# Kernel optimization log

Hardware: AMD Instinct MI355X
Metric: run time of the kernel (lower is better)

Reference implementation:

```python
import jax, jax.numpy as jnp
import numpy as np

B, S, D = 32, 512, 512
H, DH = 8, 64          # head_num, att_embedding_size
DFF = 4 * D
NEG = float(-2**32 + 1)
LN_EPS = 1e-3          # keras LayerNormalization default


def layer_norm(x, gamma, beta):
    mu = jnp.mean(x, axis=-1, keepdims=True)
    var = jnp.mean(jnp.square(x - mu), axis=-1, keepdims=True)
    return (x - mu) / jnp.sqrt(var + LN_EPS) * gamma + beta


def setup_inputs() -> dict:
    key = jax.random.key(0)
    ks = jax.random.split(key, 10)
    queries = jax.random.normal(ks[0], (B, S, D), dtype=jnp.float32)
    keys = jax.random.normal(ks[1], (B, S, D), dtype=jnp.float32)
    query_lens = jax.random.randint(ks[2], (B, 1), 1, S + 1)
    key_lens = jax.random.randint(ks[3], (B, 1), 1, S + 1)
    # learned params (TruncatedNormal stddev 0.05-ish / Glorot approximated by scaled normals)
    W_Q = jax.random.normal(ks[4], (D, D), dtype=jnp.float32) * 0.05
    W_K = jax.random.normal(ks[5], (D, D), dtype=jnp.float32) * 0.05
    W_V = jax.random.normal(ks[6], (D, D), dtype=jnp.float32) * 0.05
    fw1 = jax.random.normal(ks[7], (D, DFF), dtype=jnp.float32) * (1.0 / np.sqrt(D))
    fw2 = jax.random.normal(ks[8], (DFF, D), dtype=jnp.float32) * (1.0 / np.sqrt(DFF))
    ln_gamma = jnp.ones((D,), dtype=jnp.float32)
    ln_beta = jnp.zeros((D,), dtype=jnp.float32)
    return {"queries": queries, "keys": keys, "W_Q": W_Q, "W_K": W_K, "W_V": W_V,
            "fw1": fw1, "fw2": fw2, "ln_gamma": ln_gamma, "ln_beta": ln_beta,
            "query_lens": query_lens, "key_lens": key_lens}


def reference(queries, keys, W_Q, W_K, W_V, fw1, fw2, ln_gamma, ln_beta, query_lens, key_lens):
    # masks from sequence lengths: [B, S] float {0,1}
    pos = jnp.arange(S)
    q_mask = (pos[None, :] < query_lens).astype(queries.dtype)  # [B,S]
    k_mask = (pos[None, :] < key_lens).astype(queries.dtype)    # [B,S]

    # QKV projections, split into heads: [B,S,H,DH]
    Q = (queries @ W_Q).reshape(B, S, H, DH)
    Kp = (keys @ W_K).reshape(B, S, H, DH)
    V = (keys @ W_V).reshape(B, S, H, DH)

    # scaled dot-product scores: [B,H,Sq,Sk]
    scores = jnp.einsum('bqhd,bkhd->bhqk', Q, Kp) / jnp.sqrt(jnp.asarray(DH, queries.dtype))

    # key padding mask
    scores = jnp.where(k_mask[:, None, None, :] == 1, scores, NEG)
    # blinding: kill the diagonal (self-position)
    eye = jnp.eye(S, dtype=bool)
    scores = jnp.where(eye[None, None, :, :], NEG, scores)

    scores = scores - jnp.max(scores, axis=-1, keepdims=True)
    attn = jax.nn.softmax(scores, axis=-1)
    # query mask zeros out padded query rows (after softmax, as in source)
    attn = attn * q_mask[:, None, :, None]

    out = jnp.einsum('bhqk,bkhd->bqhd', attn, V).reshape(B, S, D)

    result = out + queries                       # use_res
    result = layer_norm(result, ln_gamma, ln_beta)  # shared ln (use_layer_norm)

    # feed-forward
    h = jax.nn.relu(result @ fw1) @ fw2
    result = result + h
    result = layer_norm(result, ln_gamma, ln_beta)

    # output_type == 'mean'
    return jnp.mean(result, axis=1, keepdims=True)  # [B,1,D]
```

## Files before the change

### kernel.cpp

```cpp
#include <hip/hip_runtime.h>

typedef unsigned short ushort_t;
typedef unsigned int uint_t;
typedef __attribute__((ext_vector_type(4))) float f32x4;
typedef __attribute__((ext_vector_type(2))) float f32x2;
typedef __attribute__((ext_vector_type(8))) short s16x8;
typedef __attribute__((ext_vector_type(8))) _Float16 f16x8;
typedef __attribute__((ext_vector_type(4))) unsigned short u16x4;

#define NEGV -60000.0f

__device__ __forceinline__ ushort_t f2bf(float f) {
  unsigned int u = __builtin_bit_cast(unsigned int, f);
  return (ushort_t)((u + 0x7fffu + ((u >> 16) & 1u)) >> 16);
}
__device__ __forceinline__ float bf2f(ushort_t h) {
  unsigned int u = ((unsigned int)h) << 16;
  return __builtin_bit_cast(float, u);
}
__device__ __forceinline__ void gload_lds16(const void* g, void* l) {
  __builtin_amdgcn_global_load_lds(
      (const __attribute__((address_space(1))) unsigned int*)g,
      (__attribute__((address_space(3))) unsigned int*)l, 16, 0, 0);
}

template<int EPI>
__global__ __launch_bounds__(256)
void gemm_bt(const ushort_t* __restrict__ A, const ushort_t* __restrict__ A2,
             int lda,
             const ushort_t* __restrict__ Bt, int ldb,
             void* __restrict__ Cv, int ldc, int K,
             long long sB, long long sC)
{
  __shared__ ushort_t As[128 * 32];
  __shared__ ushort_t Bs[128 * 32];

  const int tid = threadIdx.x;
  const int w = tid >> 6;
  const int lane = tid & 63;
  const int z = blockIdx.z;

  const ushort_t* Az = (z == 0) ? A : A2;
  const ushort_t* Bz = Bt + (size_t)z * sB;

  const int orig = blockIdx.x + gridDim.x * blockIdx.y;
  const int bx = (orig >> 3) % gridDim.x;
  const int by = (orig & 7) + 8 * ((orig >> 3) / gridDim.x);
  const int m0 = by * 128;
  const int n0 = bx * 128;

  const int wm = (w >> 1) * 64;
  const int wn = (w & 1) * 64;

  f32x4 acc[4][4];
#pragma unroll
  for (int m = 0; m < 4; ++m)
#pragma unroll
    for (int n = 0; n < 4; ++n)
      acc[m][n] = (f32x4){0.f, 0.f, 0.f, 0.f};

  const int cA0 = w * 64 + lane;
  const int cA1 = 256 + cA0;

  const int nk = K >> 5;
  for (int kt = 0; kt < nk; ++kt) {
    const int k0 = kt << 5;
    gload_lds16(Az + (size_t)(m0 + (cA0 >> 2)) * lda + (k0 + (cA0 & 3) * 8),
                As + (size_t)(w * 64) * 8);
    gload_lds16(Az + (size_t)(m0 + (cA1 >> 2)) * lda + (k0 + (cA1 & 3) * 8),
                As + (size_t)(256 + w * 64) * 8);
    gload_lds16(Bz + (size_t)(n0 + (cA0 >> 2)) * ldb + (k0 + (cA0 & 3) * 8),
                Bs + (size_t)(w * 64) * 8);
    gload_lds16(Bz + (size_t)(n0 + (cA1 >> 2)) * ldb + (k0 + (cA1 & 3) * 8),
                Bs + (size_t)(256 + w * 64) * 8);
    __syncthreads();

    s16x8 af[4], bfr[4];
#pragma unroll
    for (int m = 0; m < 4; ++m)
      af[m] = *(const s16x8*)(As + (size_t)(wm + m * 16 + (lane & 15)) * 32 +
                              ((lane >> 4) * 8));
#pragma unroll
    for (int n = 0; n < 4; ++n)
      bfr[n] = *(const s16x8*)(Bs + (size_t)(wn + n * 16 + (lane & 15)) * 32 +
                               ((lane >> 4) * 8));
#pragma unroll
    for (int m = 0; m < 4; ++m)
#pragma unroll
      for (int n = 0; n < 4; ++n)
        acc[m][n] = __builtin_amdgcn_mfma_f32_16x16x32_bf16(af[m], bfr[n],
                                                            acc[m][n], 0, 0, 0);
    __syncthreads();
  }

  const float s0 = (EPI == 4 && z == 0) ? 0.125f : 1.0f;
  char* Cz = (char*)Cv + (size_t)sC * z;
  const int r_base = (lane >> 4) * 4;
  const int c_base = lane & 15;
#pragma unroll
  for (int m = 0; m < 4; ++m)
#pragma unroll
    for (int n = 0; n < 4; ++n)
#pragma unroll
      for (int j = 0; j < 4; ++j) {
        const int rg = m0 + wm + m * 16 + r_base + j;
        const int cg = n0 + wn + n * 16 + c_base;
        float v = acc[m][n][j];
        const size_t idx = (size_t)rg * ldc + cg;
        if constexpr (EPI == 0) {
          ((float*)Cz)[idx] = v;
        } else if constexpr (EPI == 2) {
          ((ushort_t*)Cz)[idx] = f2bf(fmaxf(v, 0.f));
        } else {
          ((ushort_t*)Cz)[idx] = f2bf(v * s0);
        }
      }
}

__global__ __launch_bounds__(256, 3)
void flash_attn(const ushort_t* __restrict__ Qg, const ushort_t* __restrict__ Kg,
                const ushort_t* __restrict__ Vt, ushort_t* __restrict__ AOb,
                const int* __restrict__ qlen, const int* __restrict__ klen)
{
  __shared__ ushort_t sm[24576];
  ushort_t* PQ = sm + 16384;

  const int tid = threadIdx.x, w = tid >> 6, lane = tid & 63;
  const int fr = lane & 15, fq = lane >> 4;

  int id = blockIdx.x;
  id = (id & 7) * 128 + (id >> 3);
  const int qt = id & 3, h = (id >> 2) & 7, b = id >> 5;
  const int q0 = qt * 128;
  const int KL = klen[b], QL = qlen[b];

  if (q0 >= QL) {
#pragma unroll
    for (int i = 0; i < 8; ++i) {
      int idx = i * 256 + tid;
      int rr = idx >> 4, cc = (idx & 15) << 2;
      *(u16x4*)&AOb[((size_t)(b * 512 + q0 + rr)) * 512 + h * 64 + cc] =
          (u16x4){0, 0, 0, 0};
    }
    return;
  }

  int nt = (KL + 63) >> 6;
  if (KL == 1) nt = 8;

  const ushort_t* Qrow = Qg + ((size_t)(b * 512 + q0)) * 512 + h * 64;
  const ushort_t* Krow = Kg + ((size_t)b * 512) * 512 + h * 64;
  const ushort_t* Vrow = Vt + (((size_t)b * 8 + h) * 64) * 512;

#pragma unroll
  for (int i = 0; i < 4; ++i) {
    int s = i * 256 + tid, r = s >> 3, c = (s & 7) ^ (r & 7);
    gload_lds16(Qrow + (size_t)r * 512 + c * 8, PQ + (i * 256 + w * 64) * 8);
  }
#pragma unroll
  for (int i = 0; i < 2; ++i) {
    int s = i * 256 + tid, r = s >> 3, c = (s & 7) ^ (r & 7);
    gload_lds16(Krow + (size_t)r * 512 + c * 8, sm + (i * 256 + w * 64) * 8);
    gload_lds16(Vrow + (size_t)r * 512 + c * 8, sm + 4096 + (i * 256 + w * 64) * 8);
  }
  __syncthreads();

  s16x8 qf[2][2];
#pragma unroll
  for (int m = 0; m < 2; ++m)
#pragma unroll
    for (int kc = 0; kc < 2; ++kc) {
      int r = w * 32 + m * 16 + fr;
      qf[m][kc] = *(const s16x8*)(PQ + r * 64 + (((kc * 4 + fq) ^ (r & 7)) * 8));
    }

  float mrun[2][4], lrun[2][4];
  f32x4 oacc[2][4];
#pragma unroll
  for (int m = 0; m < 2; ++m)
#pragma unroll
    for (int j = 0; j < 4; ++j) { mrun[m][j] = -1e30f; lrun[m][j] = 0.f; }
#pragma unroll
  for (int m = 0; m < 2; ++m)
#pragma unroll
    for (int nd = 0; nd < 4; ++nd)
      oacc[m][nd] = (f32x4){0.f, 0.f, 0.f, 0.f};

  for (int t = 0; t < nt; ++t) {
    ushort_t* Kb = sm + (t & 1) * 8192;
    ushort_t* Vb = Kb + 4096;
    if (t + 1 < nt) {
      const int kv1 = (t + 1) * 64;
      ushort_t* Kn = sm + ((t + 1) & 1) * 8192;
#pragma unroll
      for (int i = 0; i < 2; ++i) {
        int s = i * 256 + tid, r = s >> 3, c = (s & 7) ^ (r & 7);
        gload_lds16(Krow + (size_t)(kv1 + r) * 512 + c * 8,
                    Kn + (i * 256 + w * 64) * 8);
        gload_lds16(Vrow + (size_t)r * 512 + kv1 + c * 8,
                    Kn + 4096 + (i * 256 + w * 64) * 8);
      }
    }
    const int kv0 = t * 64;

    f32x4 sacc[2][4];
#pragma unroll
    for (int m = 0; m < 2; ++m)
#pragma unroll
      for (int n = 0; n < 4; ++n)
        sacc[m][n] = (f32x4){0.f, 0.f, 0.f, 0.f};
#pragma unroll
    for (int n = 0; n < 4; ++n)
#pragma unroll
      for (int kc = 0; kc < 2; ++kc) {
        int r = n * 16 + fr;
        s16x8 kf = *(const s16x8*)(Kb + r * 64 + (((kc * 4 + fq) ^ (r & 7)) * 8));
        sacc[0][n] = __builtin_amdgcn_mfma_f32_16x16x32_bf16(qf[0][kc], kf, sacc[0][n], 0, 0, 0);
        sacc[1][n] = __builtin_amdgcn_mfma_f32_16x16x32_bf16(qf[1][kc], kf, sacc[1][n], 0, 0, 0);
      }

#pragma unroll
    for (int m = 0; m < 2; ++m)
#pragma unroll
      for (int j = 0; j < 4; ++j) {
        const int rl = w * 32 + m * 16 + fq * 4 + j;
        const int rg = q0 + rl;
        float sv[4];
        float tmax = -1e30f;
#pragma unroll
        for (int n = 0; n < 4; ++n) {
          int cg = kv0 + n * 16 + fr;
          float v = sacc[m][n][j];
          if (cg >= KL || cg == rg) v = NEGV;
          sv[n] = v;
          tmax = fmaxf(tmax, v);
        }
#pragma unroll
        for (int o = 1; o < 16; o <<= 1) tmax = fmaxf(tmax, __shfl_xor(tmax, o));
        const float mnew = fmaxf(mrun[m][j], tmax);
        const float sf = __expf(mrun[m][j] - mnew);
        mrun[m][j] = mnew;
        float ps = 0.f;
        _Float16* prow = (_Float16*)(PQ + rl * 64);
#pragma unroll
        for (int n = 0; n < 4; ++n) {
          float p = __expf(sv[n] - mnew);
          ps += p;
          int cl = n * 2 + (fr >> 3);
          prow[((cl ^ (rl & 7)) * 8) + (fr & 7)] = (_Float16)p;
        }
        lrun[m][j] = lrun[m][j] * sf + ps;
#pragma unroll
        for (int nd = 0; nd < 4; ++nd) oacc[m][nd][j] *= sf;
      }

#pragma unroll
    for (int kc = 0; kc < 2; ++kc) {
      s16x8 pf[2];
#pragma unroll
      for (int m = 0; m < 2; ++m) {
        int rl = w * 32 + m * 16 + fr;
        pf[m] = *(const s16x8*)(PQ + rl * 64 + (((kc * 4 + fq) ^ (rl & 7)) * 8));
      }
#pragma unroll
      for (int nd = 0; nd < 4; ++nd) {
        int d = nd * 16 + fr;
        s16x8 vf = *(const s16x8*)(Vb + d * 64 + (((kc * 4 + fq) ^ (d & 7)) * 8));
#pragma unroll
        for (int m = 0; m < 2; ++m)
          oacc[m][nd] = __builtin_amdgcn_mfma_f32_16x16x32_f16(
              __builtin_bit_cast(f16x8, pf[m]), __builtin_bit_cast(f16x8, vf),
              oacc[m][nd], 0, 0, 0);
      }
    }
    __syncthreads();
  }

#pragma unroll
  for (int m = 0; m < 2; ++m)
#pragma unroll
    for (int j = 0; j < 4; ++j) {
      float l = lrun[m][j];
#pragma unroll
      for (int o = 1; o < 16; o <<= 1) l += __shfl_xor(l, o);
      const int rg = q0 + w * 32 + m * 16 + fq * 4 + j;
      const float inv = (rg < QL) ? (1.f / l) : 0.f;
#pragma unroll
      for (int nd = 0; nd < 4; ++nd)
        AOb[((size_t)(b * 512 + rg)) * 512 + h * 64 + nd * 16 + fr] =
            f2bf(oacc[m][nd][j] * inv);
    }
}

__global__ __launch_bounds__(256) void cvt_bf16(const float* __restrict__ in,
                                                ushort_t* __restrict__ out, int n4) {
  int i = blockIdx.x * 256 + threadIdx.x;
  if (i >= n4) return;
  f32x4 v = ((const f32x4*)in)[i];
  u16x4 o;
#pragma unroll
  for (int j = 0; j < 4; ++j) o[j] = f2bf(v[j]);
  ((u16x4*)out)[i] = o;
}

__global__ __launch_bounds__(256) void transpose_cvt(const float* __restrict__ in,
                                                     ushort_t* __restrict__ out,
                                                     int R, int C) {
  __shared__ float tile[32][33];
  const int c0 = blockIdx.x * 32, r0 = blockIdx.y * 32;
  const int tx = threadIdx.x & 31, ty = threadIdx.x >> 5;
#pragma unroll
  for (int i = 0; i < 32; i += 8)
    tile[ty + i][tx] = in[(size_t)(r0 + ty + i) * C + (c0 + tx)];
  __syncthreads();
#pragma unroll
  for (int i = 0; i < 32; i += 8)
    out[(size_t)(c0 + ty + i) * R + (r0 + tx)] = f2bf(tile[tx][ty + i]);
}

__global__ __launch_bounds__(256) void build_vt(const ushort_t* __restrict__ V,
                                                ushort_t* __restrict__ Vt) {
  __shared__ ushort_t tile[64 * 65];
  const int s0 = blockIdx.x * 64, h = blockIdx.y, b = blockIdx.z;
  const int t = threadIdx.x;
#pragma unroll
  for (int i = 0; i < 16; ++i) {
    int idx = i * 256 + t;
    int sl = idx >> 6, d = idx & 63;
    tile[sl * 65 + d] = V[(size_t)(b * 512 + s0 + sl) * 512 + h * 64 + d];
  }
  __syncthreads();
  _Float16* vt = (_Float16*)Vt;
#pragma unroll
  for (int i = 0; i < 16; ++i) {
    int idx = i * 256 + t;
    int d = idx >> 6, sl = idx & 63;
    vt[((size_t)(b * 8 + h) * 64 + d) * 512 + (s0 + sl)] =
        (_Float16)bf2f(tile[sl * 65 + d]);
  }
}

__global__ __launch_bounds__(256) void ln1(const ushort_t* __restrict__ xb,
                                           const float* __restrict__ r,
                                           const float* __restrict__ g,
                                           const float* __restrict__ be,
                                           ushort_t* __restrict__ ob) {
  const int row = blockIdx.x, t = threadIdx.x;
  const size_t base = (size_t)row * 512;
  const uint_t xv = ((const uint_t*)(xb + base))[t];
  const f32x2 rv = ((const f32x2*)(r + base))[t];
  float v0 = bf2f((ushort_t)(xv & 0xffff)) + rv[0];
  float v1 = bf2f((ushort_t)(xv >> 16)) + rv[1];
  float s = v0 + v1, q = v0 * v0 + v1 * v1;
#pragma unroll
  for (int o = 32; o; o >>= 1) { s += __shfl_xor(s, o); q += __shfl_xor(q, o); }
  __shared__ float ps[4], pq[4];
  const int w = t >> 6, lane = t & 63;
  if (lane == 0) { ps[w] = s; pq[w] = q; }
  __syncthreads();
  s = ps[0] + ps[1] + ps[2] + ps[3];
  q = pq[0] + pq[1] + pq[2] + pq[3];
  const float mu = s * 0.001953125f;
  const float var = q * 0.001953125f - mu * mu;
  const float inv = 1.0f / sqrtf(var + 1e-3f);
  const float y0 = (v0 - mu) * inv * g[2 * t] + be[2 * t];
  const float y1 = (v1 - mu) * inv * g[2 * t + 1] + be[2 * t + 1];
  ((uint_t*)(ob + base))[t] = (uint_t)f2bf(y0) | ((uint_t)f2bf(y1) << 16);
}

__global__ __launch_bounds__(256) void ln2(const float* __restrict__ h2a,
                                           const float* __restrict__ h2b,
                                           const ushort_t* __restrict__ r1b,
                                           const float* __restrict__ g,
                                           const float* __restrict__ be,
                                           ushort_t* __restrict__ ob) {
  const int row = blockIdx.x, t = threadIdx.x;
  const size_t base = (size_t)row * 512;
  const f32x2 a = ((const f32x2*)(h2a + base))[t];
  const f32x2 b = ((const f32x2*)(h2b + base))[t];
  const uint_t rv = ((const uint_t*)(r1b + base))[t];
  float v0 = a[0] + b[0] + bf2f((ushort_t)(rv & 0xffff));
  float v1 = a[1] + b[1] + bf2f((ushort_t)(rv >> 16));
  float s = v0 + v1, q = v0 * v0 + v1 * v1;
#pragma unroll
  for (int o = 32; o; o >>= 1) { s += __shfl_xor(s, o); q += __shfl_xor(q, o); }
  __shared__ float ps[4], pq[4];
  const int w = t >> 6, lane = t & 63;
  if (lane == 0) { ps[w] = s; pq[w] = q; }
  __syncthreads();
  s = ps[0] + ps[1] + ps[2] + ps[3];
  q = pq[0] + pq[1] + pq[2] + pq[3];
  const float mu = s * 0.001953125f;
  const float var = q * 0.001953125f - mu * mu;
  const float inv = 1.0f / sqrtf(var + 1e-3f);
  const float y0 = (v0 - mu) * inv * g[2 * t] + be[2 * t];
  const float y1 = (v1 - mu) * inv * g[2 * t + 1] + be[2 * t + 1];
  ((uint_t*)(ob + base))[t] = (uint_t)f2bf(y0) | ((uint_t)f2bf(y1) << 16);
}

__global__ void mean_partial(const ushort_t* __restrict__ r3,
                             float* __restrict__ part) {
  const int sc = blockIdx.x, b = blockIdx.y, d = threadIdx.x;
  float s = 0.f;
#pragma unroll 4
  for (int i = 0; i < 64; ++i)
    s += bf2f(r3[(size_t)(b * 512 + sc * 64 + i) * 512 + d]);
  part[(size_t)(b * 8 + sc) * 512 + d] = s;
}
__global__ void mean_final(const float* __restrict__ part, float* __restrict__ out) {
  const int b = blockIdx.x, d = threadIdx.x;
  float s = 0.f;
#pragma unroll
  for (int i = 0; i < 8; ++i) s += part[(size_t)(b * 8 + i) * 512 + d];
  out[b * 512 + d] = s * (1.0f / 512.0f);
}

extern "C" void kernel_launch(void* const* d_in, const int* in_sizes, int n_in,
                              void* d_out, int out_size, void* d_ws, size_t ws_size,
                              hipStream_t stream) {
  (void)in_sizes; (void)n_in; (void)out_size; (void)ws_size;
  const float* queries = (const float*)d_in[0];
  const float* keys    = (const float*)d_in[1];
  const float* W_Q = (const float*)d_in[2];
  const float* W_K = (const float*)d_in[3];
  const float* W_V = (const float*)d_in[4];
  const float* fw1 = (const float*)d_in[5];
  const float* fw2 = (const float*)d_in[6];
  const float* ln_g = (const float*)d_in[7];
  const float* ln_b = (const float*)d_in[8];
  const int* qlen = (const int*)d_in[9];
  const int* klen = (const int*)d_in[10];
  float* out = (float*)d_out;

  char* ws = (char*)d_ws;
  const size_t MB = 1048576;
  ushort_t* XQ  = (ushort_t*)(ws + 0 * MB);
  ushort_t* XK  = (ushort_t*)(ws + 16 * MB);
  ushort_t* Qb  = (ushort_t*)(ws + 32 * MB);
  ushort_t* Vb  = (ushort_t*)(ws + 64 * MB);
  ushort_t* VT  = (ushort_t*)(ws + 80 * MB);
  ushort_t* AOb = (ushort_t*)(ws + 96 * MB);
  ushort_t* R1B = (ushort_t*)(ws + 112 * MB);
  ushort_t* H1  = (ushort_t*)(ws + 0 * MB);
  float*    H2  = (float*)(ws + 128 * MB);
  ushort_t* R3B = (ushort_t*)(ws + 192 * MB);
  char*     wsw = ws + 208 * MB;
  ushort_t* WQT  = (ushort_t*)(wsw);
  ushort_t* FW1T = (ushort_t*)(wsw + 3 * 524288);
  ushort_t* FW2T = (ushort_t*)(wsw + 3 * 524288 + 2097152);
  float*    PART = (float*)(wsw + 3 * 524288 + 2 * 2097152);

  cvt_bf16<<<8192, 256, 0, stream>>>(queries, XQ, 2097152);
  cvt_bf16<<<8192, 256, 0, stream>>>(keys, XK, 2097152);
  transpose_cvt<<<dim3(16, 16), 256, 0, stream>>>(W_Q, WQT, 512, 512);
  transpose_cvt<<<dim3(16, 16), 256, 0, stream>>>(W_K, WQT + 262144, 512, 512);
  transpose_cvt<<<dim3(16, 16), 256, 0, stream>>>(W_V, WQT + 524288, 512, 512);
  transpose_cvt<<<dim3(64, 16), 256, 0, stream>>>(fw1, FW1T, 512, 2048);
  transpose_cvt<<<dim3(16, 64), 256, 0, stream>>>(fw2, FW2T, 2048, 512);
  gemm_bt<4><<<dim3(4, 128, 3), 256, 0, stream>>>(
      XQ, XK, 512, WQT, 512, (void*)Qb, 512, 512, 262144, 16 * MB);
  build_vt<<<dim3(8, 8, 32), 256, 0, stream>>>(Vb, VT);
  flash_attn<<<1024, 256, 0, stream>>>(Qb, Qb + 8388608, VT, AOb, qlen, klen);
  ln1<<<16384, 256, 0, stream>>>(AOb, queries, ln_g, ln_b, R1B);
  gemm_bt<2><<<dim3(16, 128, 1), 256, 0, stream>>>(
      R1B, R1B, 512, FW1T, 512, (void*)H1, 2048, 512, 0, 0);
  gemm_bt<0><<<dim3(4, 128, 2), 256, 0, stream>>>(
      H1, H1 + 1024, 2048, FW2T, 2048, (void*)H2, 512, 1024, 1024, 32 * MB);
  ln2<<<16384, 256, 0, stream>>>(H2, H2 + 8388608, R1B, ln_g, ln_b, R3B);
  mean_partial<<<dim3(8, 32), 512, 0, stream>>>(R3B, PART);
  mean_final<<<32, 512, 0, stream>>>(PART, out);
}
```

Measured before the change: 281.4 us.

## Double-buffer GEMM LDS tiles and halve flash-attention query tile size

The bf16 GEMM now keeps two LDS stages for A and B. It issues the next k-tile's global-to-LDS loads before computing on the current one, so the load latency overlaps the MFMA work and one barrier per iteration is dropped. The flash-attention kernel moves from 128-row to 64-row query tiles, with one 16-row strip per wave. It launches twice as many blocks, uses less LDS and raises the occupancy hint from 3 to 4. Finer tiles also let more fully padded query tiles exit early, in exchange for reloading K and V more often per query row.

```diff
diff --git a/kernel.cpp b/kernel.cpp
--- a/kernel.cpp
+++ b/kernel.cpp
@@ -32,8 +32,8 @@
              void* __restrict__ Cv, int ldc, int K,
              long long sB, long long sC)
 {
-  __shared__ ushort_t As[128 * 32];
-  __shared__ ushort_t Bs[128 * 32];
+  __shared__ ushort_t As[2][128 * 32];
+  __shared__ ushort_t Bs[2][128 * 32];
 
   const int tid = threadIdx.x;
   const int w = tid >> 6;
@@ -61,28 +61,35 @@
 
   const int cA0 = w * 64 + lane;
   const int cA1 = 256 + cA0;
+  const int rA0 = cA0 >> 2, kO0 = (cA0 & 3) * 8;
+  const int rA1 = cA1 >> 2, kO1 = (cA1 & 3) * 8;
+
+  auto stage = [&](int p, int k0) {
+    gload_lds16(Az + (size_t)(m0 + rA0) * lda + (k0 + kO0),
+                As[p] + (size_t)(w * 64) * 8);
+    gload_lds16(Az + (size_t)(m0 + rA1) * lda + (k0 + kO1),
+                As[p] + (size_t)(256 + w * 64) * 8);
+    gload_lds16(Bz + (size_t)(n0 + rA0) * ldb + (k0 + kO0),
+                Bs[p] + (size_t)(w * 64) * 8);
+    gload_lds16(Bz + (size_t)(n0 + rA1) * ldb + (k0 + kO1),
+                Bs[p] + (size_t)(256 + w * 64) * 8);
+  };
 
   const int nk = K >> 5;
+  stage(0, 0);
+  __syncthreads();
   for (int kt = 0; kt < nk; ++kt) {
-    const int k0 = kt << 5;
-    gload_lds16(Az + (size_t)(m0 + (cA0 >> 2)) * lda + (k0 + (cA0 & 3) * 8),
-                As + (size_t)(w * 64) * 8);
-    gload_lds16(Az + (size_t)(m0 + (cA1 >> 2)) * lda + (k0 + (cA1 & 3) * 8),
-                As + (size_t)(256 + w * 64) * 8);
-    gload_lds16(Bz + (size_t)(n0 + (cA0 >> 2)) * ldb + (k0 + (cA0 & 3) * 8),
-                Bs + (size_t)(w * 64) * 8);
-    gload_lds16(Bz + (size_t)(n0 + (cA1 >> 2)) * ldb + (k0 + (cA1 & 3) * 8),
-                Bs + (size_t)(256 + w * 64) * 8);
-    __syncthreads();
+    const int p = kt & 1;
+    if (kt + 1 < nk) stage(p ^ 1, (kt + 1) << 5);
 
     s16x8 af[4], bfr[4];
 #pragma unroll
     for (int m = 0; m < 4; ++m)
-      af[m] = *(const s16x8*)(As + (size_t)(wm + m * 16 + (lane & 15)) * 32 +
+      af[m] = *(const s16x8*)(As[p] + (size_t)(wm + m * 16 + (lane & 15)) * 32 +
                               ((lane >> 4) * 8));
 #pragma unroll
     for (int n = 0; n < 4; ++n)
-      bfr[n] = *(const s16x8*)(Bs + (size_t)(wn + n * 16 + (lane & 15)) * 32 +
+      bfr[n] = *(const s16x8*)(Bs[p] + (size_t)(wn + n * 16 + (lane & 15)) * 32 +
                                ((lane >> 4) * 8));
 #pragma unroll
     for (int m = 0; m < 4; ++m)
@@ -117,26 +124,26 @@
       }
 }
 
-__global__ __launch_bounds__(256, 3)
+__global__ __launch_bounds__(256, 4)
 void flash_attn(const ushort_t* __restrict__ Qg, const ushort_t* __restrict__ Kg,
                 const ushort_t* __restrict__ Vt, ushort_t* __restrict__ AOb,
                 const int* __restrict__ qlen, const int* __restrict__ klen)
 {
-  __shared__ ushort_t sm[24576];
+  __shared__ ushort_t sm[20480];
   ushort_t* PQ = sm + 16384;
 
   const int tid = threadIdx.x, w = tid >> 6, lane = tid & 63;
   const int fr = lane & 15, fq = lane >> 4;
 
   int id = blockIdx.x;
-  id = (id & 7) * 128 + (id >> 3);
-  const int qt = id & 3, h = (id >> 2) & 7, b = id >> 5;
-  const int q0 = qt * 128;
+  id = (id & 7) * 256 + (id >> 3);
+  const int qt = id & 7, h = (id >> 3) & 7, b = id >> 6;
+  const int q0 = qt * 64;
   const int KL = klen[b], QL = qlen[b];
 
   if (q0 >= QL) {
 #pragma unroll
-    for (int i = 0; i < 8; ++i) {
+    for (int i = 0; i < 4; ++i) {
       int idx = i * 256 + tid;
       int rr = idx >> 4, cc = (idx & 15) << 2;
       *(u16x4*)&AOb[((size_t)(b * 512 + q0 + rr)) * 512 + h * 64 + cc] =
@@ -153,7 +160,7 @@
   const ushort_t* Vrow = Vt + (((size_t)b * 8 + h) * 64) * 512;
 
 #pragma unroll
-  for (int i = 0; i < 4; ++i) {
+  for (int i = 0; i < 2; ++i) {
     int s = i * 256 + tid, r = s >> 3, c = (s & 7) ^ (r & 7);
     gload_lds16(Qrow + (size_t)r * 512 + c * 8, PQ + (i * 256 + w * 64) * 8);
   }
@@ -165,26 +172,19 @@
   }
   __syncthreads();
 
-  s16x8 qf[2][2];
-#pragma unroll
-  for (int m = 0; m < 2; ++m)
-#pragma unroll
-    for (int kc = 0; kc < 2; ++kc) {
-      int r = w * 32 + m * 16 + fr;
-      qf[m][kc] = *(const s16x8*)(PQ + r * 64 + (((kc * 4 + fq) ^ (r & 7)) * 8));
-    }
-
-  float mrun[2][4], lrun[2][4];
-  f32x4 oacc[2][4];
-#pragma unroll
-  for (int m = 0; m < 2; ++m)
-#pragma unroll
-    for (int j = 0; j < 4; ++j) { mrun[m][j] = -1e30f; lrun[m][j] = 0.f; }
-#pragma unroll
-  for (int m = 0; m < 2; ++m)
-#pragma unroll
-    for (int nd = 0; nd < 4; ++nd)
-      oacc[m][nd] = (f32x4){0.f, 0.f, 0.f, 0.f};
+  s16x8 qf[2];
+#pragma unroll
+  for (int kc = 0; kc < 2; ++kc) {
+    int r = w * 16 + fr;
+    qf[kc] = *(const s16x8*)(PQ + r * 64 + (((kc * 4 + fq) ^ (r & 7)) * 8));
+  }
+
+  float mrun[4], lrun[4];
+  f32x4 oacc[4];
+#pragma unroll
+  for (int j = 0; j < 4; ++j) { mrun[j] = -1e30f; lrun[j] = 0.f; }
+#pragma unroll
+  for (int nd = 0; nd < 4; ++nd) oacc[nd] = (f32x4){0.f, 0.f, 0.f, 0.f};
 
   for (int t = 0; t < nt; ++t) {
     ushort_t* Kb = sm + (t & 1) * 8192;
@@ -203,93 +203,79 @@
     }
     const int kv0 = t * 64;
 
-    f32x4 sacc[2][4];
-#pragma unroll
-    for (int m = 0; m < 2; ++m)
-#pragma unroll
-      for (int n = 0; n < 4; ++n)
-        sacc[m][n] = (f32x4){0.f, 0.f, 0.f, 0.f};
+    f32x4 sacc[4];
+#pragma unroll
+    for (int n = 0; n < 4; ++n) sacc[n] = (f32x4){0.f, 0.f, 0.f, 0.f};
 #pragma unroll
     for (int n = 0; n < 4; ++n)
 #pragma unroll
       for (int kc = 0; kc < 2; ++kc) {
         int r = n * 16 + fr;
         s16x8 kf = *(const s16x8*)(Kb + r * 64 + (((kc * 4 + fq) ^ (r & 7)) * 8));
-        sacc[0][n] = __builtin_amdgcn_mfma_f32_16x16x32_bf16(qf[0][kc], kf, sacc[0][n], 0, 0, 0);
-        sacc[1][n] = __builtin_amdgcn_mfma_f32_16x16x32_bf16(qf[1][kc], kf, sacc[1][n], 0, 0, 0);
-      }
-
-#pragma unroll
-    for (int m = 0; m < 2; ++m)
-#pragma unroll
-      for (int j = 0; j < 4; ++j) {
-        const int rl = w * 32 + m * 16 + fq * 4 + j;
-        const int rg = q0 + rl;
-        float sv[4];
-        float tmax = -1e30f;
-#pragma unroll
-        for (int n = 0; n < 4; ++n) {
-          int cg = kv0 + n * 16 + fr;
-          float v = sacc[m][n][j];
-          if (cg >= KL || cg == rg) v = NEGV;
-          sv[n] = v;
-          tmax = fmaxf(tmax, v);
-        }
-#pragma unroll
-        for (int o = 1; o < 16; o <<= 1) tmax = fmaxf(tmax, __shfl_xor(tmax, o));
-        const float mnew = fmaxf(mrun[m][j], tmax);
-        const float sf = __expf(mrun[m][j] - mnew);
-        mrun[m][j] = mnew;
-        float ps = 0.f;
-        _Float16* prow = (_Float16*)(PQ + rl * 64);
-#pragma unroll
-        for (int n = 0; n < 4; ++n) {
-          float p = __expf(sv[n] - mnew);
-          ps += p;
-          int cl = n * 2 + (fr >> 3);
-          prow[((cl ^ (rl & 7)) * 8) + (fr & 7)] = (_Float16)p;
-        }
-        lrun[m][j] = lrun[m][j] * sf + ps;
-#pragma unroll
-        for (int nd = 0; nd < 4; ++nd) oacc[m][nd][j] *= sf;
-      }
+        sacc[n] = __builtin_amdgcn_mfma_f32_16x16x32_bf16(qf[kc], kf, sacc[n], 0, 0, 0);
+      }
+
+#pragma unroll
+    for (int j = 0; j < 4; ++j) {
+      const int rl = w * 16 + fq * 4 + j;
+      const int rg = q0 + rl;
+      float sv[4];
+      float tmax = -1e30f;
+#pragma unroll
+      for (int n = 0; n < 4; ++n) {
+        int cg = kv0 + n * 16 + fr;
+        float v = sacc[n][j];
+        if (cg >= KL || cg == rg) v = NEGV;
+        sv[n] = v;
+        tmax = fmaxf(tmax, v);
+      }
+#pragma unroll
+      for (int o = 1; o < 16; o <<= 1) tmax = fmaxf(tmax, __shfl_xor(tmax, o));
+      const float mnew = fmaxf(mrun[j], tmax);
+      const float sf = __expf(mrun[j] - mnew);
+      mrun[j] = mnew;
+      float ps = 0.f;
+      _Float16* prow = (_Float16*)(PQ + rl * 64);
+#pragma unroll
+      for (int n = 0; n < 4; ++n) {
+        float p = __expf(sv[n] - mnew);
+        ps += p;
+        int cl = n * 2 + (fr >> 3);
+        prow[((cl ^ (rl & 7)) * 8) + (fr & 7)] = (_Float16)p;
+      }
+      lrun[j] = lrun[j] * sf + ps;
+#pragma unroll
+      for (int nd = 0; nd < 4; ++nd) oacc[nd][j] *= sf;
+    }
 
 #pragma unroll
     for (int kc = 0; kc < 2; ++kc) {
-      s16x8 pf[2];
-#pragma unroll
-      for (int m = 0; m < 2; ++m) {
-        int rl = w * 32 + m * 16 + fr;
-        pf[m] = *(const s16x8*)(PQ + rl * 64 + (((kc * 4 + fq) ^ (rl & 7)) * 8));
-      }
+      const int rl = w * 16 + fr;
+      s16x8 pf = *(const s16x8*)(PQ + rl * 64 + (((kc * 4 + fq) ^ (rl & 7)) * 8));
 #pragma unroll
       for (int nd = 0; nd < 4; ++nd) {
         int d = nd * 16 + fr;
         s16x8 vf = *(const s16x8*)(Vb + d * 64 + (((kc * 4 + fq) ^ (d & 7)) * 8));
-#pragma unroll
-        for (int m = 0; m < 2; ++m)
-          oacc[m][nd] = __builtin_amdgcn_mfma_f32_16x16x32_f16(
-              __builtin_bit_cast(f16x8, pf[m]), __builtin_bit_cast(f16x8, vf),
-              oacc[m][nd], 0, 0, 0);
+        oacc[nd] = __builtin_amdgcn_mfma_f32_16x16x32_f16(
+            __builtin_bit_cast(f16x8, pf), __builtin_bit_cast(f16x8, vf),
+            oacc[nd], 0, 0, 0);
       }
     }
     __syncthreads();
   }
 
 #pragma unroll
-  for (int m = 0; m < 2; ++m)
-#pragma unroll
-    for (int j = 0; j < 4; ++j) {
-      float l = lrun[m][j];
-#pragma unroll
-      for (int o = 1; o < 16; o <<= 1) l += __shfl_xor(l, o);
-      const int rg = q0 + w * 32 + m * 16 + fq * 4 + j;
-      const float inv = (rg < QL) ? (1.f / l) : 0.f;
-#pragma unroll
-      for (int nd = 0; nd < 4; ++nd)
-        AOb[((size_t)(b * 512 + rg)) * 512 + h * 64 + nd * 16 + fr] =
-            f2bf(oacc[m][nd][j] * inv);
-    }
+  for (int j = 0; j < 4; ++j) {
+    float l = lrun[j];
+#pragma unroll
+    for (int o = 1; o < 16; o <<= 1) l += __shfl_xor(l, o);
+    const int rg = q0 + w * 16 + fq * 4 + j;
+    const float inv = (rg < QL) ? (1.f / l) : 0.f;
+#pragma unroll
+    for (int nd = 0; nd < 4; ++nd)
+      AOb[((size_t)(b * 512 + rg)) * 512 + h * 64 + nd * 16 + fr] =
+          f2bf(oacc[nd][j] * inv);
+  }
 }
 
 __global__ __launch_bounds__(256) void cvt_bf16(const float* __restrict__ in,
@@ -460,7 +446,7 @@
   gemm_bt<4><<<dim3(4, 128, 3), 256, 0, stream>>>(
       XQ, XK, 512, WQT, 512, (void*)Qb, 512, 512, 262144, 16 * MB);
   build_vt<<<dim3(8, 8, 32), 256, 0, stream>>>(Vb, VT);
-  flash_attn<<<1024, 256, 0, stream>>>(Qb, Qb + 8388608, VT, AOb, qlen, klen);
+  flash_attn<<<2048, 256, 0, stream>>>(Qb, Qb + 8388608, VT, AOb, qlen, klen);
   ln1<<<16384, 256, 0, stream>>>(AOb, queries, ln_g, ln_b, R1B);
   gemm_bt<2><<<dim3(16, 128, 1), 256, 0, stream>>>(
       R1B, R1B, 512, FW1T, 512, (void*)H1, 2048, 512, 0, 0);
```

Result: faster. 249.5 us (-11.3%).
